# Performance work log

Hardware: AMD Instinct MI355X
Metric: run time of the kernel (lower is better)

Reference implementation:

```python
import jax, jax.numpy as jnp
import numpy as np

G = 7          # grid_size
A = 2          # anchors_per_cell
C = 3          # num_classes
L_COORD, L_OBJ, L_NOOBJ, L_CLS = 5.0, 1.0, 0.5, 2.0


def setup_inputs() -> dict:
    key = jax.random.key(0)
    k0, k1, k2, k3, k4 = jax.random.split(key, 5)
    B, M = 32768, 20
    predictions = jax.random.normal(k0, (B, G, G, A, 5 + C), dtype=jnp.float32)
    xy1 = jax.random.uniform(k1, (B, M, 2), dtype=jnp.float32) * 0.8
    wh = jax.random.uniform(k2, (B, M, 2), dtype=jnp.float32) * 0.19 + 0.01
    target_boxes = jnp.concatenate([xy1, xy1 + wh], axis=-1)  # valid x1<x2, y1<y2
    target_labels = jax.random.randint(k3, (B, M), 0, C, dtype=jnp.int32)
    num_objs = jax.random.randint(k4, (B,), 0, M + 1, dtype=jnp.int32)
    anchors = jnp.array([[0.971, 1.7338], [3.4579, 5.1653]], dtype=jnp.float32)
    class_weights = jnp.array([1.0, 4.9, 4.8], dtype=jnp.float32)
    return dict(predictions=predictions, target_boxes=target_boxes,
                target_labels=target_labels, num_objs=num_objs,
                anchors=anchors, class_weights=class_weights)


def assign_targets(target_boxes, target_labels, num_objs, anchors, B):
    """Vectorized scatter-based replacement of the nested python assignment loop."""
    M = target_boxes.shape[1]
    x1, y1, x2, y2 = [target_boxes[..., i] for i in range(4)]  # (B,M)
    cx, cy = (x1 + x2) * 0.5, (y1 + y2) * 0.5
    w, h = x2 - x1, y2 - y1
    valid = (w > 0) & (h > 0) & (jnp.arange(M)[None, :] < num_objs[:, None])
    gi = jnp.clip(jnp.floor(cy * G).astype(jnp.int32), 0, G - 1)
    gj = jnp.clip(jnp.floor(cx * G).astype(jnp.int32), 0, G - 1)
    wg, hg = w * G, h * G
    # anchor matching IoU (width/height only), (B,M,A)
    inter = jnp.minimum(wg[..., None], anchors[:, 0]) * jnp.minimum(hg[..., None], anchors[:, 1])
    union = (wg * hg)[..., None] + anchors[:, 0] * anchors[:, 1] - inter
    best_a = jnp.argmax(inter / (union + 1e-6), axis=-1).astype(jnp.int32)  # first max = torch loop tie-break
    aw = anchors[best_a, 0]
    ah = anchors[best_a, 1]
    tx = cx * G - gj.astype(jnp.float32)
    ty = cy * G - gi.astype(jnp.float32)
    tw = jnp.log(jnp.clip(wg, 0.01, None) / (aw + 1e-6))
    th = jnp.log(jnp.clip(hg, 0.01, None) / (ah + 1e-6))
    tvals = jnp.stack([tx, ty, tw, th], axis=-1)  # (B,M,4)
    N = B * G * G * A
    bidx = jnp.arange(B, dtype=jnp.int32)[:, None]
    flat = ((bidx * G + gi) * G + gj) * A + best_a  # (B,M)
    flat = jnp.where(valid, flat, N)                # invalid -> dropped by scatter
    idx = flat.ravel()
    obj_mask = jnp.zeros((N,), jnp.float32).at[idx].set(1.0, mode='drop')
    target_bbox = jnp.zeros((N, 4), jnp.float32).at[idx].set(tvals.reshape(-1, 4), mode='drop')
    target_cls = jnp.zeros((N,), jnp.int32).at[idx].set(target_labels.ravel(), mode='drop')
    shape = (B, G, G, A)
    return obj_mask.reshape(shape), target_bbox.reshape(shape + (4,)), target_cls.reshape(shape)


def reference(predictions, target_boxes, target_labels, num_objs, anchors, class_weights):
    B = predictions.shape[0]
    pred_obj = predictions[..., 0]
    pred_bbox = predictions[..., 1:5]
    pred_cls = predictions[..., 5:]
    m, target_bbox, target_cls = assign_targets(target_boxes, target_labels, num_objs, anchors, B)
    sp = jax.nn.softplus
    # BCE-with-logits: target is 1 on obj cells, 0 on noobj cells
    loss_obj = jnp.sum(m * sp(-pred_obj))
    loss_noobj = jnp.sum((1.0 - m) * sp(pred_obj))
    # smooth L1 (beta=1), summed over obj cells
    d = pred_bbox - target_bbox
    ad = jnp.abs(d)
    sl1 = jnp.where(ad < 1.0, 0.5 * d * d, ad - 0.5)
    loss_bbox = jnp.sum(m[..., None] * sl1)
    # weighted cross entropy on obj cells
    logZ = jax.nn.logsumexpimport if False else jax.scipy.special.logsumexp(pred_cls, axis=-1)
    logit_t = jnp.take_along_axis(pred_cls, target_cls[..., None], axis=-1)[..., 0]
    loss_cls = jnp.sum(m * class_weights[target_cls] * (logZ - logit_t))
    num_pos = jnp.maximum(jnp.sum(m), 1.0)
    total = (L_COORD * loss_bbox + L_OBJ * loss_obj + L_NOOBJ * loss_noobj + L_CLS * loss_cls) / num_pos
    return total
```

## Files before the change

kernel.cpp:

```cpp
#include <hip/hip_runtime.h>


namespace {
constexpr int kG = 7;
constexpr int kA = 2;
constexpr int kM = 20;
constexpr int kCells = kG * kG * kA;
constexpr int kCh = 8;
constexpr int kNB = 32;
constexpr int kBlock = 448;
constexpr int kTgt = kNB * kM;
constexpr int kIters = (kNB * kCells) / kBlock;
}

__device__ __forceinline__ float softplus_fast(float x) {
    return fmaxf(x, 0.0f) + __logf(1.0f + __expf(-fabsf(x)));
}

__global__ __launch_bounds__(kBlock) void det_loss_fused(
    const float* __restrict__ preds,
    const float* __restrict__ tboxes,
    const int* __restrict__ tlabels,
    const int* __restrict__ nobjs,
    const float* __restrict__ anchors,
    const float* __restrict__ cweights,
    float* __restrict__ partial,
    int* __restrict__ ticket,
    float* __restrict__ out,
    int B, int nblocks)
{
    __shared__ float4 s_tv[kTgt];
    __shared__ short  s_cell[kTgt];
    __shared__ int    s_pos[kTgt];
    __shared__ int    s_nobj[kNB];
    __shared__ int    s_npos;
    __shared__ float  s_red[kBlock / 64][5];
    __shared__ int    s_last;

    const int tid = threadIdx.x;
    const int b0 = blockIdx.x * kNB;

    if (tid < kNB) {
        const int b = b0 + tid;
        s_nobj[tid] = (b < B) ? nobjs[b] : 0;
    }
    if (tid == 0) s_npos = 0;
    __syncthreads();

    const float a00 = anchors[0], a01 = anchors[1];
    const float a10 = anchors[2], a11 = anchors[3];

    for (int j = tid; j < kTgt; j += kBlock) {
        const int bl = j / kM;
        const int m  = j - bl * kM;
        short cell = -1;
        float4 tv = make_float4(0.f, 0.f, 0.f, 0.f);
        if (b0 + bl < B) {
            const float4 box = ((const float4*)tboxes)[(size_t)b0 * kM + j];
            const float x1 = box.x, y1 = box.y, x2 = box.z, y2 = box.w;
            const float cx = (x1 + x2) * 0.5f, cy = (y1 + y2) * 0.5f;
            const float w = x2 - x1, h = y2 - y1;
            if (w > 0.f && h > 0.f && m < s_nobj[bl]) {
                const int gi = min(max((int)floorf(cy * (float)kG), 0), kG - 1);
                const int gj = min(max((int)floorf(cx * (float)kG), 0), kG - 1);
                const float wg = w * (float)kG, hg = h * (float)kG;
                const float i0 = fminf(wg, a00) * fminf(hg, a01);
                const float u0 = wg * hg + a00 * a01 - i0;
                const float r0 = i0 / (u0 + 1e-6f);
                const float i1 = fminf(wg, a10) * fminf(hg, a11);
                const float u1 = wg * hg + a10 * a11 - i1;
                const float r1 = i1 / (u1 + 1e-6f);
                const int a = (r1 > r0) ? 1 : 0;
                const float aw = a ? a10 : a00;
                const float ah = a ? a11 : a01;
                tv.x = cx * (float)kG - (float)gj;
                tv.y = cy * (float)kG - (float)gi;
                tv.z = __logf(fmaxf(wg, 0.01f) / (aw + 1e-6f));
                tv.w = __logf(fmaxf(hg, 0.01f) / (ah + 1e-6f));
                cell = (short)(bl * kCells + (gi * kG + gj) * kA + a);
            }
        }
        s_cell[j] = cell;
        s_tv[j] = tv;
    }
    __syncthreads();

    for (int j = tid; j < kTgt; j += kBlock) {
        const short c = s_cell[j];
        if (c >= 0) {
            const int bl = j / kM;
            const int m  = j - bl * kM;
            bool win = true;
            for (int m2 = m + 1; m2 < kM; ++m2) {
                if (s_cell[bl * kM + m2] == c) { win = false; break; }
            }
            if (win) {
                const int idx = atomicAdd(&s_npos, 1);
                s_pos[idx] = (j << 16) | (int)c;
            }
        }
    }
    __syncthreads();

    float accO = 0.f, accN = 0.f, accB = 0.f, accC = 0.f;
    const float* __restrict__ pblk = preds + (size_t)b0 * kCells * kCh;
    if (b0 + kNB <= B) {
        #pragma unroll
        for (int k = 0; k < kIters; ++k) {
            const float po = pblk[(size_t)(tid + k * kBlock) * kCh];
            accN += softplus_fast(po);
        }
    } else {
        const int ncell = (B - b0) * kCells;
        for (int i = tid; i < ncell; i += kBlock)
            accN += softplus_fast(pblk[(size_t)i * kCh]);
    }

    const int np = s_npos;
    const float cw0 = cweights[0], cw1 = cweights[1], cw2 = cweights[2];
    for (int t = tid; t < np; t += kBlock) {
        const int pk = s_pos[t];
        const int j  = pk >> 16;
        const int ci = pk & 0xFFFF;
        const float4* pc = (const float4*)(pblk + (size_t)ci * kCh);
        const float4 p0 = pc[0];
        const float4 p1 = pc[1];
        const float spp = softplus_fast(p0.x);
        accN -= spp;
        accO += spp - p0.x;
        const float4 tv = s_tv[j];
        float d, ad;
        d = p0.y - tv.x; ad = fabsf(d); accB += (ad < 1.f) ? 0.5f * d * d : ad - 0.5f;
        d = p0.z - tv.y; ad = fabsf(d); accB += (ad < 1.f) ? 0.5f * d * d : ad - 0.5f;
        d = p0.w - tv.z; ad = fabsf(d); accB += (ad < 1.f) ? 0.5f * d * d : ad - 0.5f;
        d = p1.x - tv.w; ad = fabsf(d); accB += (ad < 1.f) ? 0.5f * d * d : ad - 0.5f;
        const int lab = tlabels[(size_t)b0 * kM + j];
        const float c0 = p1.y, c1 = p1.z, c2 = p1.w;
        const float mx = fmaxf(c0, fmaxf(c1, c2));
        const float lse = mx + __logf(__expf(c0 - mx) + __expf(c1 - mx) + __expf(c2 - mx));
        const float logit = (lab == 0) ? c0 : ((lab == 1) ? c1 : c2);
        const float cwv   = (lab == 0) ? cw0 : ((lab == 1) ? cw1 : cw2);
        accC += cwv * (lse - logit);
    }

    float vals[4] = {accO, accN, accB, accC};
    #pragma unroll
    for (int k = 0; k < 4; ++k) {
        float v = vals[k];
        #pragma unroll
        for (int off = 32; off > 0; off >>= 1) v += __shfl_down(v, off, 64);
        vals[k] = v;
    }
    const int wave = tid >> 6;
    const int lane = tid & 63;
    if (lane == 0) {
        #pragma unroll
        for (int k = 0; k < 4; ++k) s_red[wave][k] = vals[k];
    }
    __syncthreads();

    if (tid == 0) {
        float t[4];
        #pragma unroll
        for (int k = 0; k < 4; ++k) {
            float s = 0.f;
            #pragma unroll
            for (int w = 0; w < kBlock / 64; ++w) s += s_red[w][k];
            t[k] = s;
        }
        atomicExch(&partial[(size_t)0 * nblocks + blockIdx.x], t[0]);
        atomicExch(&partial[(size_t)1 * nblocks + blockIdx.x], t[1]);
        atomicExch(&partial[(size_t)2 * nblocks + blockIdx.x], t[2]);
        atomicExch(&partial[(size_t)3 * nblocks + blockIdx.x], t[3]);
        atomicExch(&partial[(size_t)4 * nblocks + blockIdx.x], (float)np);
        __threadfence();
        const int done = atomicAdd(ticket, 1);
        s_last = (done == nblocks - 1) ? 1 : 0;
    }
    __syncthreads();

    if (s_last) {
        float v[5] = {0.f, 0.f, 0.f, 0.f, 0.f};
        for (int i = tid; i < nblocks; i += kBlock) {
            #pragma unroll
            for (int k = 0; k < 5; ++k)
                v[k] += atomicAdd(&partial[(size_t)k * nblocks + i], 0.0f);
        }
        #pragma unroll
        for (int k = 0; k < 5; ++k) {
            float x = v[k];
            #pragma unroll
            for (int off = 32; off > 0; off >>= 1) x += __shfl_down(x, off, 64);
            v[k] = x;
        }
        if (lane == 0) {
            #pragma unroll
            for (int k = 0; k < 5; ++k) s_red[wave][k] = v[k];
        }
        __syncthreads();
        if (tid == 0) {
            float t[5];
            #pragma unroll
            for (int k = 0; k < 5; ++k) {
                float s = 0.f;
                #pragma unroll
                for (int w = 0; w < kBlock / 64; ++w) s += s_red[w][k];
                t[k] = s;
            }
            const float npv = fmaxf(t[4], 1.0f);
            out[0] = (5.0f * t[2] + 1.0f * t[0] + 0.5f * t[1] + 2.0f * t[3]) / npv;
        }
    }
}

extern "C" void kernel_launch(void* const* d_in, const int* in_sizes, int n_in,
                              void* d_out, int out_size, void* d_ws, size_t ws_size,
                              hipStream_t stream) {
    const float* preds    = (const float*)d_in[0];
    const float* tboxes   = (const float*)d_in[1];
    const int*   tlabels  = (const int*)d_in[2];
    const int*   nobjs    = (const int*)d_in[3];
    const float* anchors  = (const float*)d_in[4];
    const float* cweights = (const float*)d_in[5];
    float* out = (float*)d_out;

    const int B = in_sizes[0] / (kCells * kCh);
    const int blocks = (B + kNB - 1) / kNB;

    float* partial = (float*)d_ws;
    int*   ticket  = (int*)(partial + (size_t)5 * blocks);

    hipMemsetAsync(ticket, 0, sizeof(int), stream);
    det_loss_fused<<<blocks, kBlock, 0, stream>>>(
        preds, tboxes, tlabels, nobjs, anchors, cweights, partial, ticket, out, B, blocks);
}
```

Before: 219.7 us.

## Stream predictions as contiguous float4 chunks and split final reduction into separate kernel

The noobj pass now reads every prediction as contiguous float4 chunks, two per cell, and only even threads evaluate softplus on the objectness lane. Before, each thread did a strided scalar load every 32 bytes. The last-block ticket scheme with atomics and a memset is replaced by plain stores of per-block partials plus a second single-block reduce kernel. The loads become fully coalesced but all 32 bytes per cell are now fetched, though those sectors were probably fetched by the strided loads anyway. Half the threads do no softplus work, and the change adds a second kernel launch while dropping the memset and atomics.

```diff
diff --git a/kernel.cpp b/kernel.cpp
--- a/kernel.cpp
+++ b/kernel.cpp
@@ -10,14 +10,15 @@
 constexpr int kNB = 32;
 constexpr int kBlock = 448;
 constexpr int kTgt = kNB * kM;
-constexpr int kIters = (kNB * kCells) / kBlock;
+constexpr int kChunks = kNB * kCells * 2;
+constexpr int kIters = kChunks / kBlock;
 }
 
 __device__ __forceinline__ float softplus_fast(float x) {
     return fmaxf(x, 0.0f) + __logf(1.0f + __expf(-fabsf(x)));
 }
 
-__global__ __launch_bounds__(kBlock) void det_loss_fused(
+__global__ __launch_bounds__(kBlock) void det_loss_main(
     const float* __restrict__ preds,
     const float* __restrict__ tboxes,
     const int* __restrict__ tlabels,
@@ -25,17 +26,14 @@
     const float* __restrict__ anchors,
     const float* __restrict__ cweights,
     float* __restrict__ partial,
-    int* __restrict__ ticket,
-    float* __restrict__ out,
-    int B, int nblocks)
+    int B)
 {
     __shared__ float4 s_tv[kTgt];
     __shared__ short  s_cell[kTgt];
     __shared__ int    s_pos[kTgt];
     __shared__ int    s_nobj[kNB];
     __shared__ int    s_npos;
-    __shared__ float  s_red[kBlock / 64][5];
-    __shared__ int    s_last;
+    __shared__ float  s_red[kBlock / 64][4];
 
     const int tid = threadIdx.x;
     const int b0 = blockIdx.x * kNB;
@@ -104,16 +102,21 @@
 
     float accO = 0.f, accN = 0.f, accB = 0.f, accC = 0.f;
     const float* __restrict__ pblk = preds + (size_t)b0 * kCells * kCh;
+    const float4* __restrict__ pblk4 = (const float4*)pblk;
     if (b0 + kNB <= B) {
+        const bool hasObj = (tid & 1) == 0;
         #pragma unroll
         for (int k = 0; k < kIters; ++k) {
-            const float po = pblk[(size_t)(tid + k * kBlock) * kCh];
-            accN += softplus_fast(po);
+            const float4 v = pblk4[(size_t)(tid + k * kBlock)];
+            if (hasObj) accN += softplus_fast(v.x);
         }
     } else {
-        const int ncell = (B - b0) * kCells;
-        for (int i = tid; i < ncell; i += kBlock)
-            accN += softplus_fast(pblk[(size_t)i * kCh]);
+        const int nchunk = (B - b0) * kCells * 2;
+        const bool hasObj = (tid & 1) == 0;
+        for (int i = tid; i < nchunk; i += kBlock) {
+            const float4 v = pblk4[(size_t)i];
+            if (hasObj) accN += softplus_fast(v.x);
+        }
     }
 
     const int np = s_npos;
@@ -158,58 +161,54 @@
         for (int k = 0; k < 4; ++k) s_red[wave][k] = vals[k];
     }
     __syncthreads();
-
     if (tid == 0) {
-        float t[4];
+        const int nb = gridDim.x;
         #pragma unroll
         for (int k = 0; k < 4; ++k) {
+            float t = 0.f;
+            #pragma unroll
+            for (int w = 0; w < kBlock / 64; ++w) t += s_red[w][k];
+            partial[(size_t)k * nb + blockIdx.x] = t;
+        }
+        partial[(size_t)4 * nb + blockIdx.x] = (float)np;
+    }
+}
+
+__global__ __launch_bounds__(256) void det_loss_reduce(
+    const float* __restrict__ partial, int nblocks, float* __restrict__ out)
+{
+    __shared__ float s_red[4][5];
+    const int tid = threadIdx.x;
+    float v[5] = {0.f, 0.f, 0.f, 0.f, 0.f};
+    for (int i = tid; i < nblocks; i += 256) {
+        #pragma unroll
+        for (int k = 0; k < 5; ++k) v[k] += partial[(size_t)k * nblocks + i];
+    }
+    #pragma unroll
+    for (int k = 0; k < 5; ++k) {
+        float x = v[k];
+        #pragma unroll
+        for (int off = 32; off > 0; off >>= 1) x += __shfl_down(x, off, 64);
+        v[k] = x;
+    }
+    const int wave = tid >> 6;
+    const int lane = tid & 63;
+    if (lane == 0) {
+        #pragma unroll
+        for (int k = 0; k < 5; ++k) s_red[wave][k] = v[k];
+    }
+    __syncthreads();
+    if (tid == 0) {
+        float t[5];
+        #pragma unroll
+        for (int k = 0; k < 5; ++k) {
             float s = 0.f;
             #pragma unroll
-            for (int w = 0; w < kBlock / 64; ++w) s += s_red[w][k];
+            for (int w = 0; w < 4; ++w) s += s_red[w][k];
             t[k] = s;
         }
-        atomicExch(&partial[(size_t)0 * nblocks + blockIdx.x], t[0]);
-        atomicExch(&partial[(size_t)1 * nblocks + blockIdx.x], t[1]);
-        atomicExch(&partial[(size_t)2 * nblocks + blockIdx.x], t[2]);
-        atomicExch(&partial[(size_t)3 * nblocks + blockIdx.x], t[3]);
-        atomicExch(&partial[(size_t)4 * nblocks + blockIdx.x], (float)np);
-        __threadfence();
-        const int done = atomicAdd(ticket, 1);
-        s_last = (done == nblocks - 1) ? 1 : 0;
-    }
-    __syncthreads();
-
-    if (s_last) {
-        float v[5] = {0.f, 0.f, 0.f, 0.f, 0.f};
-        for (int i = tid; i < nblocks; i += kBlock) {
-            #pragma unroll
-            for (int k = 0; k < 5; ++k)
-                v[k] += atomicAdd(&partial[(size_t)k * nblocks + i], 0.0f);
-        }
-        #pragma unroll
-        for (int k = 0; k < 5; ++k) {
-            float x = v[k];
-            #pragma unroll
-            for (int off = 32; off > 0; off >>= 1) x += __shfl_down(x, off, 64);
-            v[k] = x;
-        }
-        if (lane == 0) {
-            #pragma unroll
-            for (int k = 0; k < 5; ++k) s_red[wave][k] = v[k];
-        }
-        __syncthreads();
-        if (tid == 0) {
-            float t[5];
-            #pragma unroll
-            for (int k = 0; k < 5; ++k) {
-                float s = 0.f;
-                #pragma unroll
-                for (int w = 0; w < kBlock / 64; ++w) s += s_red[w][k];
-                t[k] = s;
-            }
-            const float npv = fmaxf(t[4], 1.0f);
-            out[0] = (5.0f * t[2] + 1.0f * t[0] + 0.5f * t[1] + 2.0f * t[3]) / npv;
-        }
+        const float npv = fmaxf(t[4], 1.0f);
+        out[0] = (5.0f * t[2] + 1.0f * t[0] + 0.5f * t[1] + 2.0f * t[3]) / npv;
     }
 }
 
@@ -223,14 +222,12 @@
     const float* anchors  = (const float*)d_in[4];
     const float* cweights = (const float*)d_in[5];
     float* out = (float*)d_out;
+    float* partial = (float*)d_ws;
 
     const int B = in_sizes[0] / (kCells * kCh);
     const int blocks = (B + kNB - 1) / kNB;
 
-    float* partial = (float*)d_ws;
-    int*   ticket  = (int*)(partial + (size_t)5 * blocks);
-
-    hipMemsetAsync(ticket, 0, sizeof(int), stream);
-    det_loss_fused<<<blocks, kBlock, 0, stream>>>(
-        preds, tboxes, tlabels, nobjs, anchors, cweights, partial, ticket, out, B, blocks);
-}
+    det_loss_main<<<blocks, kBlock, 0, stream>>>(
+        preds, tboxes, tlabels, nobjs, anchors, cweights, partial, B);
+    det_loss_reduce<<<1, 256, 0, stream>>>(partial, blocks, out);
+}
```

Measured after the change: 184.2 us, median of 2. -16.2%, faster.
